# Kernel tuning notes

Hardware: AMD Instinct MI355X
Metric: run time of the kernel (lower is better)

Reference implementation:

```python
import jax, jax.numpy as jnp
import numpy as np

N_NODES = 50000
N_EDGES = 600000
F_IN = 128
DIM_H = 256
N_CLASSES = 40
BN_EPS = 1e-5


def setup_inputs() -> dict:
    key = jax.random.key(0)
    ks = jax.random.split(key, 10)
    x = jax.random.normal(ks[0], (N_NODES, F_IN), dtype=jnp.float32)
    edge_index = jax.random.randint(ks[1], (2, N_EDGES), 0, N_NODES, dtype=jnp.int64)
    s1 = 1.0 / np.sqrt(F_IN)
    s2 = 1.0 / np.sqrt(DIM_H)
    W1 = jax.random.uniform(ks[2], (F_IN, DIM_H), jnp.float32, -s1, s1)
    b1 = jax.random.uniform(ks[3], (DIM_H,), jnp.float32, -s1, s1)
    gamma = jnp.ones((DIM_H,), jnp.float32)
    beta = jnp.zeros((DIM_H,), jnp.float32)
    W2 = jax.random.uniform(ks[4], (DIM_H, DIM_H), jnp.float32, -s2, s2)
    b2 = jax.random.uniform(ks[5], (DIM_H,), jnp.float32, -s2, s2)
    Wlin = jax.random.uniform(ks[6], (DIM_H, N_CLASSES), jnp.float32, -s2, s2)
    blin = jax.random.uniform(ks[7], (N_CLASSES,), jnp.float32, -s2, s2)
    return {"x": x, "edge_index": edge_index, "W1": W1, "b1": b1,
            "gamma": gamma, "beta": beta, "W2": W2, "b2": b2,
            "Wlin": Wlin, "blin": blin}


def reference(x, edge_index, W1, b1, gamma, beta, W2, b2, Wlin, blin):
    src, dst = edge_index[0], edge_index[1]
    # GIN sum aggregation: agg[i] = sum_{(j->i)} x[j]; eps = 0 (default)
    agg = jax.ops.segment_sum(x[src], dst, num_segments=N_NODES)  # [N, F_IN]
    h = x + agg
    # MLP: Linear -> BatchNorm1d (training-mode batch stats) -> ReLU -> Linear -> ReLU
    h = h @ W1 + b1                               # [N, DIM_H]
    mean = jnp.mean(h, axis=0)
    var = jnp.var(h, axis=0)                      # biased, as torch BN uses for normalization
    h = (h - mean) * jax.lax.rsqrt(var + BN_EPS) * gamma + beta
    h = jax.nn.relu(h)
    h = jax.nn.relu(h @ W2 + b2)                  # MLP final ReLU; outer x.relu() is idempotent
    return h @ Wlin + blin                        # [N, N_CLASSES]
```

## Files before the change

### kernel.cpp

```cpp
#include <hip/hip_runtime.h>

#define F_IN 128
#define DIM_H 256
#define N_CLASSES 40
#define BN_EPS 1e-5f
#define M_PAD 50176

typedef short bf16x8 __attribute__((ext_vector_type(8)));
typedef float f32x4 __attribute__((ext_vector_type(4)));

__device__ __forceinline__ unsigned short f2bf(float f) {
    union { float f; unsigned u; } v; v.f = f;
    unsigned r = v.u + 0x7fff + ((v.u >> 16) & 1);
    return (unsigned short)(r >> 16);
}
__device__ __forceinline__ float bf2f(unsigned short u) {
    union { unsigned u; float f; } v; v.u = ((unsigned)u) << 16;
    return v.f;
}
__device__ __forceinline__ float4 bf2f4(ushort4 u) {
    return make_float4(bf2f(u.x), bf2f(u.y), bf2f(u.z), bf2f(u.w));
}

__global__ void hist_kernel(const int* __restrict__ dst, int* __restrict__ hist, int nE) {
    int e = blockIdx.x * blockDim.x + threadIdx.x;
    if (e >= nE) return;
    atomicAdd(&hist[dst[e]], 1);
}

__global__ void scan_blocks_kernel(const int* __restrict__ hist,
                                   int* __restrict__ blockSums, int M) {
    __shared__ int lds[256];
    int t = threadIdx.x;
    int i = blockIdx.x * 256 + t;
    lds[t] = (i < M) ? hist[i] : 0;
    __syncthreads();
    for (int off = 128; off > 0; off >>= 1) {
        if (t < off) lds[t] += lds[t + off];
        __syncthreads();
    }
    if (t == 0) blockSums[blockIdx.x] = lds[0];
}

__global__ void scan_final_kernel(const int* __restrict__ hist,
                                  const int* __restrict__ blockSums,
                                  int* __restrict__ start, int M, int nE) {
    __shared__ int lds[256];
    int t = threadIdx.x;
    lds[t] = (t < blockIdx.x) ? blockSums[t] : 0;
    __syncthreads();
    for (int o = 128; o > 0; o >>= 1) {
        if (t < o) lds[t] += lds[t + o];
        __syncthreads();
    }
    int off = lds[0];
    __syncthreads();
    int i = blockIdx.x * 256 + t;
    int orig = (i < M) ? hist[i] : 0;
    lds[t] = orig;
    __syncthreads();
    for (int o = 1; o < 256; o <<= 1) {
        int v = (t >= o) ? lds[t - o] : 0;
        __syncthreads();
        lds[t] += v;
        __syncthreads();
    }
    if (i < M) start[i] = off + lds[t] - orig;
    if (blockIdx.x == 0 && t == 0) start[M] = nE;
}

__global__ void fill_kernel(const int* __restrict__ src, const int* __restrict__ dst,
                            const int* __restrict__ start, int* __restrict__ cursor,
                            int* __restrict__ order, int nE) {
    int e = blockIdx.x * blockDim.x + threadIdx.x;
    if (e >= nE) return;
    int d = dst[e];
    int pos = start[d] + atomicAdd(&cursor[d], 1);
    order[pos] = src[e];
}

__global__ void prep_kernel(const float* __restrict__ x, unsigned short* __restrict__ xb,
                            const float* __restrict__ W1, const float* __restrict__ W2,
                            const float* __restrict__ Wl,
                            unsigned short* __restrict__ W1t,
                            unsigned short* __restrict__ W2t,
                            unsigned short* __restrict__ Wlt,
                            int* __restrict__ histz,
                            int XQ, int ZQ) {
    int idx = blockIdx.x * 256 + threadIdx.x;
    if (idx < XQ) {
        float4 v = ((const float4*)x)[idx];
        ushort4 o;
        o.x = f2bf(v.x); o.y = f2bf(v.y); o.z = f2bf(v.z); o.w = f2bf(v.w);
        ((ushort4*)xb)[idx] = o;
        return;
    }
    int j = idx - XQ;
    if (j < 32768) {
        int n = j >> 7, k = j & 127;
        W1t[j] = f2bf(W1[k * DIM_H + n]);
    } else if (j < 32768 + 65536) {
        int i = j - 32768;
        int n = i >> 8, k = i & 255;
        W2t[i] = f2bf(W2[k * DIM_H + n]);
    } else if (j < 32768 + 65536 + 16384) {
        int i = j - 98304;
        int n = i >> 8, k = i & 255;
        Wlt[i] = f2bf((n < N_CLASSES) ? Wl[k * N_CLASSES + n] : 0.f);
    } else if (j < 114688 + 0 + 1) {
    }
    int z = j - 114688;
    if (z >= 0 && z < ZQ) {
        ((int4*)histz)[z] = make_int4(0, 0, 0, 0);
    }
}

__global__ void bn_reduce_kernel(const float* __restrict__ partials, int R,
                                 const float* __restrict__ gamma,
                                 const float* __restrict__ beta,
                                 float* __restrict__ scale,
                                 float* __restrict__ shift, int M) {
    __shared__ float ls[256], lss[256];
    int c = blockIdx.x, t = threadIdx.x;
    float s = 0.f, ss = 0.f;
    for (int r = t; r < R; r += 256) {
        s += partials[(long)r * 512 + c];
        ss += partials[(long)r * 512 + 256 + c];
    }
    ls[t] = s; lss[t] = ss;
    __syncthreads();
    for (int o = 128; o > 0; o >>= 1) {
        if (t < o) { ls[t] += ls[t + o]; lss[t] += lss[t + o]; }
        __syncthreads();
    }
    if (t == 0) {
        float inv = 1.0f / (float)M;
        float mean = ls[0] * inv;
        float var = lss[0] * inv - mean * mean;
        float sc = gamma[c] * rsqrtf(var + BN_EPS);
        scale[c] = sc;
        shift[c] = beta[c] - mean * sc;
    }
}

__global__ __launch_bounds__(256, 4) void gin_gemm1_kernel(
    const unsigned short* __restrict__ xb,
    const int* __restrict__ order, const int* __restrict__ start,
    const unsigned short* __restrict__ W1t, const float* __restrict__ b1,
    unsigned short* __restrict__ h1, float* __restrict__ partials, int M) {
    constexpr int K = F_IN, S = K / 32;
    constexpr int PA = 136;
    constexpr int PB = 40;
    constexpr int PH = 264;
    __shared__ __align__(16) unsigned short lds[64 * PA + 256 * PB];
    unsigned short* At = lds;
    unsigned short* Bs = lds + 64 * PA;
    unsigned short* h1t = lds;

    int tid = threadIdx.x;
    int wave = tid >> 6, lane = tid & 63;
    int l15 = lane & 15, q = lane >> 4;
    int wn = wave;
    long row0 = (long)blockIdx.x * 64;

    bf16x8 br[4];
    auto loadB = [&](int s) {
#pragma unroll
        for (int i = 0; i < 4; ++i) {
            int ch = tid + i * 256;
            int m = ch >> 2, c = ch & 3;
            br[i] = *(const bf16x8*)(W1t + m * K + s * 32 + c * 8);
        }
    };
    auto writeB = [&]() {
#pragma unroll
        for (int i = 0; i < 4; ++i) {
            int ch = tid + i * 256;
            int m = ch >> 2, c = ch & 3;
            *(bf16x8*)(&Bs[m * PB + c * 8]) = br[i];
        }
    };

    loadB(0);

    {
        int hw = tid >> 5, lane32 = tid & 31;
        const ushort4* xv = (const ushort4*)xb;
        for (int rr = 0; rr < 8; ++rr) {
            int r = rr * 8 + hw;
            long node = row0 + r;
            float4 a0 = make_float4(0.f, 0.f, 0.f, 0.f);
            float4 a1 = a0, a2 = a0, a3 = a0;
            if (node < M) {
                a0 = bf2f4(xv[node * 32 + lane32]);
                int e0 = start[node], e1 = start[node + 1];
                int e = e0;
                for (; e + 4 <= e1; e += 4) {
                    int s0 = order[e], s1 = order[e + 1], s2 = order[e + 2], s3 = order[e + 3];
                    float4 v0 = bf2f4(xv[(size_t)s0 * 32 + lane32]);
                    float4 v1 = bf2f4(xv[(size_t)s1 * 32 + lane32]);
                    float4 v2 = bf2f4(xv[(size_t)s2 * 32 + lane32]);
                    float4 v3 = bf2f4(xv[(size_t)s3 * 32 + lane32]);
                    a0.x += v0.x; a0.y += v0.y; a0.z += v0.z; a0.w += v0.w;
                    a1.x += v1.x; a1.y += v1.y; a1.z += v1.z; a1.w += v1.w;
                    a2.x += v2.x; a2.y += v2.y; a2.z += v2.z; a2.w += v2.w;
                    a3.x += v3.x; a3.y += v3.y; a3.z += v3.z; a3.w += v3.w;
                }
                for (; e < e1; ++e) {
                    float4 v = bf2f4(xv[(size_t)order[e] * 32 + lane32]);
                    a1.x += v.x; a1.y += v.y; a1.z += v.z; a1.w += v.w;
                }
            }
            float4 t;
            t.x = (a0.x + a1.x) + (a2.x + a3.x);
            t.y = (a0.y + a1.y) + (a2.y + a3.y);
            t.z = (a0.z + a1.z) + (a2.z + a3.z);
            t.w = (a0.w + a1.w) + (a2.w + a3.w);
            ushort4 o;
            o.x = f2bf(t.x); o.y = f2bf(t.y); o.z = f2bf(t.z); o.w = f2bf(t.w);
            *(ushort4*)(&At[r * PA + lane32 * 4]) = o;
        }
    }
    writeB();
    __syncthreads();

    f32x4 acc[4][4] = {};
#pragma unroll
    for (int s = 0; s < S; ++s) {
        if (s + 1 < S) loadB(s + 1);
        bf16x8 af[4], bfr[4];
#pragma unroll
        for (int mt = 0; mt < 4; ++mt)
            af[mt] = *(const bf16x8*)(&At[(mt * 16 + l15) * PA + s * 32 + q * 8]);
#pragma unroll
        for (int nt = 0; nt < 4; ++nt)
            bfr[nt] = *(const bf16x8*)(&Bs[(wn * 64 + nt * 16 + l15) * PB + q * 8]);
#pragma unroll
        for (int mt = 0; mt < 4; ++mt)
#pragma unroll
            for (int nt = 0; nt < 4; ++nt)
                acc[mt][nt] = __builtin_amdgcn_mfma_f32_16x16x32_bf16(
                    af[mt], bfr[nt], acc[mt][nt], 0, 0, 0);
        __syncthreads();
        if (s + 1 < S) { writeB(); __syncthreads(); }
    }

#pragma unroll
    for (int nt = 0; nt < 4; ++nt) {
        int col = wn * 64 + nt * 16 + l15;
        float b = b1[col];
        float s = 0.f, ss = 0.f;
#pragma unroll
        for (int mt = 0; mt < 4; ++mt) {
#pragma unroll
            for (int r = 0; r < 4; ++r) {
                long row = row0 + mt * 16 + q * 4 + r;
                float v = acc[mt][nt][r] + b;
                if (row < M) { s += v; ss += v * v; }
                h1t[(mt * 16 + q * 4 + r) * PH + col] = f2bf(v);
            }
        }
        s += __shfl_xor(s, 16, 64);  s += __shfl_xor(s, 32, 64);
        ss += __shfl_xor(ss, 16, 64); ss += __shfl_xor(ss, 32, 64);
        if (lane < 16) {
            partials[(long)blockIdx.x * 512 + col] = s;
            partials[(long)blockIdx.x * 512 + 256 + col] = ss;
        }
    }
    __syncthreads();
    {
        int srow = tid >> 2, scol = (tid & 3) * 64;
        unsigned short* dst = h1 + (row0 + srow) * DIM_H + scol;
        const unsigned short* srcp = &h1t[srow * PH + scol];
#pragma unroll
        for (int j = 0; j < 8; ++j)
            *(bf16x8*)(dst + j * 8) = *(const bf16x8*)(srcp + j * 8);
    }
}

__global__ __launch_bounds__(512, 4) void gemm23_kernel(
    const unsigned short* __restrict__ h1, const unsigned short* __restrict__ W2t,
    const float* __restrict__ b2,
    const float* __restrict__ scale, const float* __restrict__ shift,
    const unsigned short* __restrict__ Wlt, const float* __restrict__ blin,
    float* __restrict__ out, int M) {
    constexpr int S = 8;
    constexpr int PA = 40, PB = 40, PH = 264;
    constexpr int STAGE = 128 * PA + 256 * PB;
    __shared__ __align__(16) unsigned short lds[128 * PH];
    unsigned short* h2t = lds;

    int tid = threadIdx.x;
    int wave = tid >> 6, lane = tid & 63;
    int wm = wave >> 2, wn = wave & 3;
    int l15 = lane & 15, q = lane >> 4;
    long row0 = (long)blockIdx.x * 128;

    int am = tid >> 2, ac = tid & 3;
    bf16x8 ar, br[2];
    auto loadAB = [&](int s) {
        ar = *(const bf16x8*)(h1 + (row0 + am) * DIM_H + s * 32 + ac * 8);
#pragma unroll
        for (int i = 0; i < 2; ++i) {
            int ch = tid + i * 512;
            int m = ch >> 2, c = ch & 3;
            br[i] = *(const bf16x8*)(W2t + m * DIM_H + s * 32 + c * 8);
        }
    };
    auto writeAB = [&](int s, int buf) {
        unsigned short* As = lds + buf * STAGE;
        unsigned short* Bs = As + 128 * PA;
        {
            int kb = s * 32 + ac * 8;
            float4 sc0 = *(const float4*)(scale + kb);
            float4 sc1 = *(const float4*)(scale + kb + 4);
            float4 sh0 = *(const float4*)(shift + kb);
            float4 sh1 = *(const float4*)(shift + kb + 4);
            float scv[8] = {sc0.x, sc0.y, sc0.z, sc0.w, sc1.x, sc1.y, sc1.z, sc1.w};
            float shv[8] = {sh0.x, sh0.y, sh0.z, sh0.w, sh1.x, sh1.y, sh1.z, sh1.w};
            bf16x8 v = ar;
#pragma unroll
            for (int j = 0; j < 8; ++j) {
                float f = bf2f((unsigned short)v[j]);
                f = fmaxf(f * scv[j] + shv[j], 0.f);
                v[j] = (short)f2bf(f);
            }
            *(bf16x8*)(&As[am * PA + ac * 8]) = v;
        }
#pragma unroll
        for (int i = 0; i < 2; ++i) {
            int ch = tid + i * 512;
            int m = ch >> 2, c = ch & 3;
            *(bf16x8*)(&Bs[m * PB + c * 8]) = br[i];
        }
    };

    f32x4 acc[4][4] = {};
    loadAB(0);
    writeAB(0, 0);
#pragma unroll
    for (int s = 0; s < S; ++s) {
        if (s + 1 < S) loadAB(s + 1);
        __syncthreads();
        const unsigned short* As = lds + (s & 1) * STAGE;
        const unsigned short* Bs = As + 128 * PA;
        bf16x8 af[4], bfr[4];
#pragma unroll
        for (int mt = 0; mt < 4; ++mt)
            af[mt] = *(const bf16x8*)(&As[(wm * 64 + mt * 16 + l15) * PA + q * 8]);
#pragma unroll
        for (int nt = 0; nt < 4; ++nt)
            bfr[nt] = *(const bf16x8*)(&Bs[(wn * 64 + nt * 16 + l15) * PB + q * 8]);
#pragma unroll
        for (int mt = 0; mt < 4; ++mt)
#pragma unroll
            for (int nt = 0; nt < 4; ++nt)
                acc[mt][nt] = __builtin_amdgcn_mfma_f32_16x16x32_bf16(
                    af[mt], bfr[nt], acc[mt][nt], 0, 0, 0);
        if (s + 1 < S) writeAB(s + 1, (s + 1) & 1);
    }
    __syncthreads();

#pragma unroll
    for (int nt = 0; nt < 4; ++nt) {
        int colL = wn * 64 + nt * 16 + l15;
        float b = b2[colL];
#pragma unroll
        for (int mt = 0; mt < 4; ++mt)
#pragma unroll
            for (int r = 0; r < 4; ++r) {
                int rowL = wm * 64 + mt * 16 + q * 4 + r;
                h2t[rowL * PH + colL] = f2bf(fmaxf(acc[mt][nt][r] + b, 0.f));
            }
    }
    __syncthreads();

    f32x4 acc3[3] = {};
#pragma unroll
    for (int s = 0; s < 8; ++s) {
        bf16x8 a3 = *(const bf16x8*)(&h2t[(wave * 16 + l15) * PH + s * 32 + q * 8]);
#pragma unroll
        for (int nt = 0; nt < 3; ++nt) {
            bf16x8 b3 = *(const bf16x8*)(Wlt + (nt * 16 + l15) * 256 + s * 32 + q * 8);
            acc3[nt] = __builtin_amdgcn_mfma_f32_16x16x32_bf16(a3, b3, acc3[nt], 0, 0, 0);
        }
    }
#pragma unroll
    for (int nt = 0; nt < 3; ++nt) {
        int col = nt * 16 + l15;
        if (col < N_CLASSES) {
            float b = blin[col];
#pragma unroll
            for (int r = 0; r < 4; ++r) {
                long row = row0 + wave * 16 + q * 4 + r;
                if (row < M) out[row * N_CLASSES + col] = acc3[nt][r] + b;
            }
        }
    }
}

extern "C" void kernel_launch(void* const* d_in, const int* in_sizes, int n_in,
                              void* d_out, int out_size, void* d_ws, size_t ws_size,
                              hipStream_t stream) {
    const float* x     = (const float*)d_in[0];
    const int*   ei    = (const int*)d_in[1];
    const float* W1    = (const float*)d_in[2];
    const float* b1    = (const float*)d_in[3];
    const float* gamma = (const float*)d_in[4];
    const float* beta  = (const float*)d_in[5];
    const float* W2    = (const float*)d_in[6];
    const float* b2    = (const float*)d_in[7];
    const float* Wlin  = (const float*)d_in[8];
    const float* blin  = (const float*)d_in[9];
    float* out = (float*)d_out;

    int M  = in_sizes[0] / F_IN;
    int nE = in_sizes[1] / 2;
    const int* srcIdx = ei;
    const int* dstIdx = ei + nE;
    int nB = (M + 255) / 256;
    int gy1 = (M + 63) / 64;
    int gy23 = (M + 127) / 128;
    int XQ = M * 32;
    int ZQ = 2 * M / 4;

    unsigned short* h1bf  = (unsigned short*)d_ws;
    unsigned short* xb    = h1bf + (size_t)M_PAD * DIM_H;
    unsigned short* W1t   = xb + (size_t)M_PAD * F_IN;
    unsigned short* W2t   = W1t + DIM_H * F_IN;
    unsigned short* Wlt   = W2t + DIM_H * DIM_H;
    float*          partials = (float*)(Wlt + 64 * DIM_H);
    float*          scale = partials + (size_t)800 * 512;
    float*          shift = scale + DIM_H;
    int*            hist  = (int*)(shift + DIM_H);
    int*            cursor= hist + M;
    int*            start = cursor + M;
    int*            blockSums = start + (M + 1);
    int*            order = blockSums + 256;

    int tB = 256;
    prep_kernel<<<(XQ + 114688 + ZQ + 255) / 256, 256, 0, stream>>>(
        x, xb, W1, W2, Wlin, W1t, W2t, Wlt, hist, XQ, ZQ);
    hist_kernel<<<(nE + tB - 1) / tB, tB, 0, stream>>>(dstIdx, hist, nE);
    scan_blocks_kernel<<<nB, 256, 0, stream>>>(hist, blockSums, M);
    scan_final_kernel<<<nB, 256, 0, stream>>>(hist, blockSums, start, M, nE);
    fill_kernel<<<(nE + tB - 1) / tB, tB, 0, stream>>>(srcIdx, dstIdx, start, cursor, order, nE);

    gin_gemm1_kernel<<<gy1, 256, 0, stream>>>(xb, order, start, W1t, b1, h1bf, partials, M);
    bn_reduce_kernel<<<DIM_H, 256, 0, stream>>>(partials, gy1, gamma, beta, scale, shift, M);
    gemm23_kernel<<<gy23, 512, 0, stream>>>(h1bf, W2t, b2, scale, shift, Wlt, blin, out, M);
}
```

Before: 241.5 us.

## Aggregate block edges with LDS float atomics and load W1 fragments directly

Neighbour aggregation now walks the block's whole contiguous edge range, shared across all waves, instead of going one destination row per half-wave. Each edge's source index and local destination row are packed into one order word, and contributions are summed into an fp32 LDS tile with atomics. This balances uneven degrees across waves but adds LDS atomic traffic. The W1 tile is no longer staged through LDS; B fragments are loaded straight from global into registers with one-step prefetch, which removes two barriers per k-step. The 16-bit source packing only works while the node count stays below 65536.

Result: slower. 713.3 us (+195.3%).

```diff
diff --git a/kernel.cpp b/kernel.cpp
--- a/kernel.cpp
+++ b/kernel.cpp
@@ -76,7 +76,7 @@
     if (e >= nE) return;
     int d = dst[e];
     int pos = start[d] + atomicAdd(&cursor[d], 1);
-    order[pos] = src[e];
+    order[pos] = (src[e] & 0xFFFF) | ((d & 63) << 16);
 }
 
 __global__ void prep_kernel(const float* __restrict__ x, unsigned short* __restrict__ xb,
@@ -107,11 +107,9 @@
         int i = j - 98304;
         int n = i >> 8, k = i & 255;
         Wlt[i] = f2bf((n < N_CLASSES) ? Wl[k * N_CLASSES + n] : 0.f);
-    } else if (j < 114688 + 0 + 1) {
-    }
-    int z = j - 114688;
-    if (z >= 0 && z < ZQ) {
-        ((int4*)histz)[z] = make_int4(0, 0, 0, 0);
+    } else {
+        int z = j - 114688;
+        if (z >= 0 && z < ZQ) ((int4*)histz)[z] = make_int4(0, 0, 0, 0);
     }
 }
 
@@ -148,14 +146,11 @@
     const int* __restrict__ order, const int* __restrict__ start,
     const unsigned short* __restrict__ W1t, const float* __restrict__ b1,
     unsigned short* __restrict__ h1, float* __restrict__ partials, int M) {
-    constexpr int K = F_IN, S = K / 32;
-    constexpr int PA = 136;
-    constexpr int PB = 40;
+    constexpr int S = F_IN / 32;
+    constexpr int PF = 132;
     constexpr int PH = 264;
-    __shared__ __align__(16) unsigned short lds[64 * PA + 256 * PB];
-    unsigned short* At = lds;
-    unsigned short* Bs = lds + 64 * PA;
-    unsigned short* h1t = lds;
+    __shared__ __align__(16) float Af[64 * PF];
+    unsigned short* h1t = (unsigned short*)Af;
 
     int tid = threadIdx.x;
     int wave = tid >> 6, lane = tid & 63;
@@ -163,87 +158,94 @@
     int wn = wave;
     long row0 = (long)blockIdx.x * 64;
 
-    bf16x8 br[4];
-    auto loadB = [&](int s) {
-#pragma unroll
-        for (int i = 0; i < 4; ++i) {
-            int ch = tid + i * 256;
-            int m = ch >> 2, c = ch & 3;
-            br[i] = *(const bf16x8*)(W1t + m * K + s * 32 + c * 8);
-        }
-    };
-    auto writeB = [&]() {
-#pragma unroll
-        for (int i = 0; i < 4; ++i) {
-            int ch = tid + i * 256;
-            int m = ch >> 2, c = ch & 3;
-            *(bf16x8*)(&Bs[m * PB + c * 8]) = br[i];
-        }
-    };
-
-    loadB(0);
+    {
+        int row = tid >> 2, seg = tid & 3;
+        long node = row0 + row;
+        float* dst = &Af[row * PF + seg * 32];
+        if (node < M) {
+            const unsigned short* srcp = xb + node * F_IN + seg * 32;
+#pragma unroll
+            for (int c = 0; c < 4; ++c) {
+                ushort4 u = *(const ushort4*)(srcp + c * 8);
+                ushort4 u2 = *(const ushort4*)(srcp + c * 8 + 4);
+                float4 f0 = bf2f4(u), f1 = bf2f4(u2);
+                *(float4*)(dst + c * 8) = f0;
+                *(float4*)(dst + c * 8 + 4) = f1;
+            }
+        } else {
+#pragma unroll
+            for (int c = 0; c < 8; ++c)
+                *(float4*)(dst + c * 4) = make_float4(0.f, 0.f, 0.f, 0.f);
+        }
+    }
+    __syncthreads();
 
     {
         int hw = tid >> 5, lane32 = tid & 31;
+        int rend = (int)min(row0 + 64, (long)M);
+        int estart = start[row0], eend = start[rend];
         const ushort4* xv = (const ushort4*)xb;
-        for (int rr = 0; rr < 8; ++rr) {
-            int r = rr * 8 + hw;
-            long node = row0 + r;
-            float4 a0 = make_float4(0.f, 0.f, 0.f, 0.f);
-            float4 a1 = a0, a2 = a0, a3 = a0;
-            if (node < M) {
-                a0 = bf2f4(xv[node * 32 + lane32]);
-                int e0 = start[node], e1 = start[node + 1];
-                int e = e0;
-                for (; e + 4 <= e1; e += 4) {
-                    int s0 = order[e], s1 = order[e + 1], s2 = order[e + 2], s3 = order[e + 3];
-                    float4 v0 = bf2f4(xv[(size_t)s0 * 32 + lane32]);
-                    float4 v1 = bf2f4(xv[(size_t)s1 * 32 + lane32]);
-                    float4 v2 = bf2f4(xv[(size_t)s2 * 32 + lane32]);
-                    float4 v3 = bf2f4(xv[(size_t)s3 * 32 + lane32]);
-                    a0.x += v0.x; a0.y += v0.y; a0.z += v0.z; a0.w += v0.w;
-                    a1.x += v1.x; a1.y += v1.y; a1.z += v1.z; a1.w += v1.w;
-                    a2.x += v2.x; a2.y += v2.y; a2.z += v2.z; a2.w += v2.w;
-                    a3.x += v3.x; a3.y += v3.y; a3.z += v3.z; a3.w += v3.w;
-                }
-                for (; e < e1; ++e) {
-                    float4 v = bf2f4(xv[(size_t)order[e] * 32 + lane32]);
-                    a1.x += v.x; a1.y += v.y; a1.z += v.z; a1.w += v.w;
-                }
-            }
-            float4 t;
-            t.x = (a0.x + a1.x) + (a2.x + a3.x);
-            t.y = (a0.y + a1.y) + (a2.y + a3.y);
-            t.z = (a0.z + a1.z) + (a2.z + a3.z);
-            t.w = (a0.w + a1.w) + (a2.w + a3.w);
-            ushort4 o;
-            o.x = f2bf(t.x); o.y = f2bf(t.y); o.z = f2bf(t.z); o.w = f2bf(t.w);
-            *(ushort4*)(&At[r * PA + lane32 * 4]) = o;
-        }
-    }
-    writeB();
+        int e = estart + hw;
+        for (; e + 24 < eend; e += 32) {
+            int o0 = order[e], o1 = order[e + 8], o2 = order[e + 16], o3 = order[e + 24];
+            float4 v0 = bf2f4(xv[(size_t)(o0 & 0xFFFF) * 32 + lane32]);
+            float4 v1 = bf2f4(xv[(size_t)(o1 & 0xFFFF) * 32 + lane32]);
+            float4 v2 = bf2f4(xv[(size_t)(o2 & 0xFFFF) * 32 + lane32]);
+            float4 v3 = bf2f4(xv[(size_t)(o3 & 0xFFFF) * 32 + lane32]);
+            float* p0 = &Af[(o0 >> 16) * PF + lane32 * 4];
+            float* p1 = &Af[(o1 >> 16) * PF + lane32 * 4];
+            float* p2 = &Af[(o2 >> 16) * PF + lane32 * 4];
+            float* p3 = &Af[(o3 >> 16) * PF + lane32 * 4];
+            atomicAdd(p0 + 0, v0.x); atomicAdd(p0 + 1, v0.y); atomicAdd(p0 + 2, v0.z); atomicAdd(p0 + 3, v0.w);
+            atomicAdd(p1 + 0, v1.x); atomicAdd(p1 + 1, v1.y); atomicAdd(p1 + 2, v1.z); atomicAdd(p1 + 3, v1.w);
+            atomicAdd(p2 + 0, v2.x); atomicAdd(p2 + 1, v2.y); atomicAdd(p2 + 2, v2.z); atomicAdd(p2 + 3, v2.w);
+            atomicAdd(p3 + 0, v3.x); atomicAdd(p3 + 1, v3.y); atomicAdd(p3 + 2, v3.z); atomicAdd(p3 + 3, v3.w);
+        }
+        for (; e < eend; e += 8) {
+            int o0 = order[e];
+            float4 v0 = bf2f4(xv[(size_t)(o0 & 0xFFFF) * 32 + lane32]);
+            float* p0 = &Af[(o0 >> 16) * PF + lane32 * 4];
+            atomicAdd(p0 + 0, v0.x); atomicAdd(p0 + 1, v0.y);
+            atomicAdd(p0 + 2, v0.z); atomicAdd(p0 + 3, v0.w);
+        }
+    }
     __syncthreads();
 
     f32x4 acc[4][4] = {};
+    bf16x8 bcur[4], bnxt[4];
+#pragma unroll
+    for (int nt = 0; nt < 4; ++nt)
+        bcur[nt] = *(const bf16x8*)(W1t + (wn * 64 + nt * 16 + l15) * F_IN + q * 8);
 #pragma unroll
     for (int s = 0; s < S; ++s) {
-        if (s + 1 < S) loadB(s + 1);
-        bf16x8 af[4], bfr[4];
-#pragma unroll
-        for (int mt = 0; mt < 4; ++mt)
-            af[mt] = *(const bf16x8*)(&At[(mt * 16 + l15) * PA + s * 32 + q * 8]);
-#pragma unroll
-        for (int nt = 0; nt < 4; ++nt)
-            bfr[nt] = *(const bf16x8*)(&Bs[(wn * 64 + nt * 16 + l15) * PB + q * 8]);
+        if (s + 1 < S) {
+#pragma unroll
+            for (int nt = 0; nt < 4; ++nt)
+                bnxt[nt] = *(const bf16x8*)(W1t + (wn * 64 + nt * 16 + l15) * F_IN + (s + 1) * 32 + q * 8);
+        }
+        bf16x8 af[4];
+#pragma unroll
+        for (int mt = 0; mt < 4; ++mt) {
+            const float* ap = &Af[(mt * 16 + l15) * PF + s * 32 + q * 8];
+            float4 lo = *(const float4*)ap;
+            float4 hi = *(const float4*)(ap + 4);
+            bf16x8 a;
+            a[0] = (short)f2bf(lo.x); a[1] = (short)f2bf(lo.y);
+            a[2] = (short)f2bf(lo.z); a[3] = (short)f2bf(lo.w);
+            a[4] = (short)f2bf(hi.x); a[5] = (short)f2bf(hi.y);
+            a[6] = (short)f2bf(hi.z); a[7] = (short)f2bf(hi.w);
+            af[mt] = a;
+        }
 #pragma unroll
         for (int mt = 0; mt < 4; ++mt)
 #pragma unroll
             for (int nt = 0; nt < 4; ++nt)
                 acc[mt][nt] = __builtin_amdgcn_mfma_f32_16x16x32_bf16(
-                    af[mt], bfr[nt], acc[mt][nt], 0, 0, 0);
-        __syncthreads();
-        if (s + 1 < S) { writeB(); __syncthreads(); }
-    }
+                    af[mt], bcur[nt], acc[mt][nt], 0, 0, 0);
+#pragma unroll
+        for (int nt = 0; nt < 4; ++nt) bcur[nt] = bnxt[nt];
+    }
+    __syncthreads();
 
 #pragma unroll
     for (int nt = 0; nt < 4; ++nt) {
```
